# Optimization experiments

Hardware: AMD Instinct MI355X
Metric: run time of the kernel (lower is better)

## Reference

```python
import jax, jax.numpy as jnp
import numpy as np

C = 512
B, W, H = 16, 64, 64
K = 128


def setup_inputs() -> dict:
    key = jax.random.key(0)
    ks = jax.random.split(key, 17)
    s = 0.02
    inp = {
        "x1": jax.random.normal(ks[0], (B, C, W, H), jnp.float32),
        "y1": jax.random.normal(ks[1], (B, K, C), jnp.float32),
        "x2": jax.random.normal(ks[2], (B, C, W, H), jnp.float32),
        "y2": jax.random.normal(ks[3], (B, K, C), jnp.float32),
        # 1x1 conv weights stored as [out, in]
        "wq1": jax.random.normal(ks[4], (C // 4, C), jnp.float32) * s,
        "bq1": jnp.zeros((C // 4,), jnp.float32),
        "wq2": jax.random.normal(ks[5], (C // 4, C), jnp.float32) * s,
        "bq2": jnp.zeros((C // 4,), jnp.float32),
        "wk1": jax.random.normal(ks[6], (C // 2, C), jnp.float32) * s,
        "bk1": jnp.zeros((C // 2,), jnp.float32),
        "wk2": jax.random.normal(ks[7], (C // 2, C), jnp.float32) * s,
        "bk2": jnp.zeros((C // 2,), jnp.float32),
        "wv1": jax.random.normal(ks[8], (C, C), jnp.float32) * s,
        "bv1": jnp.zeros((C,), jnp.float32),
        "wv2": jax.random.normal(ks[9], (C, C), jnp.float32) * s,
        "bv2": jnp.zeros((C,), jnp.float32),
        "scale": jnp.ones((1,), jnp.float32) * 0.5,  # nn.Parameter(zeros) would kill grads; nonzero for testing
    }
    return inp


def reference(x1, y1, x2, y2, wq1, bq1, wq2, bq2, wk1, bk1, wk2, bk2,
              wv1, bv1, wv2, bv2, scale):
    b, c, w, h = x1.shape
    n = w * h
    # 1x1 convs == channel-wise linear maps
    q1 = jnp.einsum('bcwh,dc->bdwh', x1, wq1) + bq1[None, :, None, None]
    q2 = jnp.einsum('bcwh,dc->bdwh', x2, wq2) + bq2[None, :, None, None]
    # concat along channels -> [B, C/2, N] -> [B, N, C/2]
    q = jnp.concatenate([q1, q2], axis=1).reshape(b, c // 2, n).transpose(0, 2, 1)
    k1 = y1 @ wk1.T + bk1  # [B, K, C/2]
    k2 = y2 @ wk2.T + bk2
    v1 = y1 @ wv1.T + bv1  # [B, K, C]
    v2 = y2 @ wv2.T + bv2
    e1 = jnp.einsum('bnd,bkd->bnk', q, k1)  # [B, N, K]
    e2 = jnp.einsum('bnd,bkd->bnk', q, k2)
    attn = jax.nn.softmax(jnp.abs(e1 - e2), axis=-1)
    # out = value^T @ attn^T : [B, C, N]
    o1 = jnp.einsum('bkc,bnk->bcn', v1, attn).reshape(b, c, w, h)
    o2 = jnp.einsum('bkc,bnk->bcn', v2, attn).reshape(b, c, w, h)
    out1 = scale[0] * o1 + x1
    out2 = scale[0] * o2 + x2
    return out1, out2
```

## Files before the change

kernel.cpp:

```cpp
#include <hip/hip_runtime.h>

typedef unsigned short u16;
typedef __attribute__((ext_vector_type(8))) short short8v;
typedef __attribute__((ext_vector_type(4))) float floatx4;

#define B_ 16
#define C_ 512
#define N_ 4096
#define K_ 128

__device__ __forceinline__ float bf2f(u16 u) {
    unsigned int x = ((unsigned int)u) << 16;
    return __builtin_bit_cast(float, x);
}
__device__ __forceinline__ u16 f2bf(float f) {
    unsigned int u = __builtin_bit_cast(unsigned int, f);
    u = u + 0x7FFFu + ((u >> 16) & 1u);
    return (u16)(u >> 16);
}
__device__ __forceinline__ void gload_lds16(const u16* g, u16* l) {
    __builtin_amdgcn_global_load_lds(
        (const __attribute__((address_space(1))) void*)g,
        (__attribute__((address_space(3))) void*)l, 16, 0, 0);
}

__global__ void conv_all(const float* __restrict__ y1, const float* __restrict__ y2,
                         const float* __restrict__ wk1, const float* __restrict__ wk2,
                         const float* __restrict__ wv1, const float* __restrict__ wv2,
                         const float* __restrict__ wq1, const float* __restrict__ wq2,
                         u16* y1b, u16* y2b, u16* wk1b, u16* wk2b, u16* wv1b, u16* wv2b,
                         u16* wq1t, u16* wq2t) {
    int tid = blockIdx.x * 256 + threadIdx.x;
    const int SY = B_ * K_ * C_;
    const int SWK = 256 * 512;
    const int SWV = 512 * 512;
    const int SQ = 128 * 512;
    int base = 2*SY + 2*SWK + 2*SWV;
    if (tid < base) {
        const float* src; u16* dst; int off;
        if (tid < SY)                 { src = y1;  dst = y1b;  off = tid; }
        else if (tid < 2*SY)          { src = y2;  dst = y2b;  off = tid - SY; }
        else if (tid < 2*SY+SWK)      { src = wk1; dst = wk1b; off = tid - 2*SY; }
        else if (tid < 2*SY+2*SWK)    { src = wk2; dst = wk2b; off = tid - 2*SY - SWK; }
        else if (tid < 2*SY+2*SWK+SWV){ src = wv1; dst = wv1b; off = tid - 2*SY - 2*SWK; }
        else                          { src = wv2; dst = wv2b; off = tid - 2*SY - 2*SWK - SWV; }
        dst[off] = f2bf(src[off]);
    } else {
        int e = tid - base;
        const float* s = (e >= SQ) ? wq2 : wq1;
        u16* d = (e >= SQ) ? wq2t : wq1t;
        e &= (SQ - 1);
        int dd = e >> 9;
        int c = e & 511;
        d[c * 128 + dd] = f2bf(s[dd * 512 + c]);
    }
}

__global__ void gemm_gkgv(const u16* __restrict__ y1b, const u16* __restrict__ y2b,
                          const u16* __restrict__ wk1b, const u16* __restrict__ wk2b,
                          const u16* __restrict__ wv1b, const u16* __restrict__ wv2b,
                          const float* __restrict__ bk1, const float* __restrict__ bk2,
                          const float* __restrict__ bv1, const float* __restrict__ bv2,
                          u16* k1b, u16* k2b, u16* vt1, u16* vt2) {
    int l = threadIdx.x;
    int id = blockIdx.x;
    const u16 *A, *Bt; const float* bias; u16* outp;
    int m0, n0, po; bool bias_m;
    if (id < 256) {
        int bx = id & 1, by = (id >> 1) & 3, z = id >> 3;
        int b = z >> 1, which = z & 1;
        A = (which ? y2b : y1b) + (size_t)b * K_ * C_;
        Bt = which ? wk2b : wk1b;
        bias = which ? bk2 : bk1;
        outp = (which ? k2b : k1b) + (size_t)b * K_ * 256;
        m0 = bx * 64; n0 = by * 64; po = 256; bias_m = false;
    } else {
        int id2 = id - 256;
        int bx = id2 & 7, by = (id2 >> 3) & 1, z = id2 >> 4;
        int b = z >> 1, which = z & 1;
        A = which ? wv2b : wv1b;
        Bt = (which ? y2b : y1b) + (size_t)b * K_ * C_;
        bias = which ? bv2 : bv1;
        outp = (which ? vt2 : vt1) + (size_t)b * C_ * K_;
        m0 = bx * 64; n0 = by * 64; po = 128; bias_m = true;
    }
    floatx4 acc[4][4] = {};
    for (int ch = 0; ch < 16; ++ch) {
        int koff = ch * 32 + (l >> 4) * 8;
        short8v a[4], wv[4];
#pragma unroll
        for (int mf = 0; mf < 4; ++mf) a[mf] = *(const short8v*)(A + (size_t)(m0 + mf*16 + (l & 15)) * 512 + koff);
#pragma unroll
        for (int nf = 0; nf < 4; ++nf) wv[nf] = *(const short8v*)(Bt + (size_t)(n0 + nf*16 + (l & 15)) * 512 + koff);
#pragma unroll
        for (int mf = 0; mf < 4; ++mf)
#pragma unroll
            for (int nf = 0; nf < 4; ++nf)
                acc[mf][nf] = __builtin_amdgcn_mfma_f32_16x16x32_bf16(a[mf], wv[nf], acc[mf][nf], 0, 0, 0);
    }
#pragma unroll
    for (int mf = 0; mf < 4; ++mf)
#pragma unroll
        for (int nf = 0; nf < 4; ++nf)
#pragma unroll
            for (int rg = 0; rg < 4; ++rg) {
                int m = m0 + mf*16 + (l >> 4)*4 + rg;
                int n = n0 + nf*16 + (l & 15);
                outp[(size_t)m * po + n] = f2bf(acc[mf][nf][rg] + (bias_m ? bias[m] : bias[n]));
            }
}

__global__ void kd_sub(const u16* __restrict__ k1b, const u16* __restrict__ k2b,
                       u16* kd) {
    int tid = blockIdx.x * 256 + threadIdx.x;
    kd[tid] = f2bf(bf2f(k1b[tid]) - bf2f(k2b[tid]));
}

__global__ void ebd_k(const u16* __restrict__ kd,
                      const float* __restrict__ bq1, const float* __restrict__ bq2,
                      float* ebd) {
    int tid = blockIdx.x * 256 + threadIdx.x;
    const u16* kb = kd + (size_t)tid * 256;
    float s = 0.f;
    for (int d = 0; d < 128; ++d) s += bq1[d] * bf2f(kb[d]);
    for (int d = 0; d < 128; ++d) s += bq2[d] * bf2f(kb[128 + d]);
    ebd[tid] = s;
}

__global__ void gemm_gkk(const u16* __restrict__ kd,
                         const u16* __restrict__ wq1t, const u16* __restrict__ wq2t,
                         u16* kkd1, u16* kkd2) {
    int l = threadIdx.x;
    int z = blockIdx.z; int b = z >> 1; int which = z & 1;
    const u16* A = kd + (size_t)b * K_ * 256 + which * 128;
    const u16* Wt = which ? wq2t : wq1t;
    u16* outp = (which ? kkd2 : kkd1) + (size_t)b * K_ * C_;
    int m0 = blockIdx.x * 64, n0 = blockIdx.y * 64;
    floatx4 acc[4][4] = {};
    for (int ch = 0; ch < 4; ++ch) {
        int koff = ch * 32 + (l >> 4) * 8;
        short8v a[4], wv[4];
#pragma unroll
        for (int mf = 0; mf < 4; ++mf) a[mf] = *(const short8v*)(A + (size_t)(m0 + mf*16 + (l & 15)) * 256 + koff);
#pragma unroll
        for (int nf = 0; nf < 4; ++nf) wv[nf] = *(const short8v*)(Wt + (size_t)(n0 + nf*16 + (l & 15)) * 128 + koff);
#pragma unroll
        for (int mf = 0; mf < 4; ++mf)
#pragma unroll
            for (int nf = 0; nf < 4; ++nf)
                acc[mf][nf] = __builtin_amdgcn_mfma_f32_16x16x32_bf16(a[mf], wv[nf], acc[mf][nf], 0, 0, 0);
    }
#pragma unroll
    for (int mf = 0; mf < 4; ++mf)
#pragma unroll
        for (int nf = 0; nf < 4; ++nf)
#pragma unroll
            for (int rg = 0; rg < 4; ++rg) {
                int m = m0 + mf*16 + (l >> 4)*4 + rg;
                int n = n0 + nf*16 + (l & 15);
                outp[(size_t)m * C_ + n] = f2bf(acc[mf][nf][rg]);
            }
}

__global__ __launch_bounds__(256, 2)
void e_attn(const float* __restrict__ x1, const float* __restrict__ x2,
            const u16* __restrict__ kkd1, const u16* __restrict__ kkd2,
            const float* __restrict__ ebd, u16* __restrict__ attnb) {
    __shared__ u16 xT[2][128 * 64];
    __shared__ u16 kkS[2][128 * 64];

    int id = blockIdx.x;
    int sw = ((id & 7) << 6) | (id >> 3);
    int b = sw >> 5;
    int n0 = (sw & 31) * 128;
    int t = threadIdx.x, w = t >> 6, l = t & 63;

    const float* xs[2] = { x1 + (size_t)b * C_ * N_, x2 + (size_t)b * C_ * N_ };
    const u16* kkp[2] = { kkd1 + (size_t)b * K_ * C_, kkd2 + (size_t)b * K_ * C_ };

    floatx4 ed[2][8] = {};

    float xA0[16], xA1[16], xB0[16], xB1[16];

    auto SLOADX = [&](int s, float (&v0)[16], float (&v1)[16]) {
        int h = s >> 3, c0 = (s & 7) * 64;
        const float* xp = xs[h] + (size_t)(c0 + w * 16) * N_ + n0 + 2 * l;
#pragma unroll
        for (int j = 0; j < 16; ++j) {
            float2 f = *(const float2*)(xp + (size_t)j * N_);
            v0[j] = f.x; v1[j] = f.y;
        }
    };
    auto KLDS = [&](int s, int buf) {
        int h = s >> 3, c0 = (s & 7) * 64;
        const u16* kp = kkp[h] + c0;
#pragma unroll
        for (int i = 0; i < 4; ++i) {
            int gi = i * 256 + t;
            int key = gi >> 3, gp = gi & 7;
            gload_lds16(kp + (size_t)key * 512 + (gp ^ (key & 7)) * 8,
                        &kkS[buf][(i * 256 + w * 64) * 8]);
        }
    };
    auto SWRITEX = [&](int buf, float (&v0)[16], float (&v1)[16]) {
        short8v p00, p01, p10, p11;
#pragma unroll
        for (int j = 0; j < 8; ++j) {
            p00[j] = (short)f2bf(v0[j]);  p01[j] = (short)f2bf(v0[j + 8]);
            p10[j] = (short)f2bf(v1[j]);  p11[j] = (short)f2bf(v1[j + 8]);
        }
        u16* xb = xT[buf];
        int row0 = 2 * l, sz = l & 7;
        *(short8v*)&xb[row0 * 64 + 8 * ((w * 2) ^ sz)] = p00;
        *(short8v*)&xb[row0 * 64 + 8 * ((w * 2 + 1) ^ sz)] = p01;
        *(short8v*)&xb[(row0 + 1) * 64 + 8 * ((w * 2) ^ sz)] = p10;
        *(short8v*)&xb[(row0 + 1) * 64 + 8 * ((w * 2 + 1) ^ sz)] = p11;
    };
    auto COMPUTE = [&](int buf) {
        u16* xb = xT[buf]; u16* kb = kkS[buf];
#pragma unroll
        for (int cc = 0; cc < 2; ++cc) {
            short8v a[2];
#pragma unroll
            for (int mf = 0; mf < 2; ++mf) {
                int row = w * 32 + mf * 16 + (l & 15);
                int g = cc * 4 + (l >> 4);
                a[mf] = *(const short8v*)&xb[row * 64 + 8 * (g ^ ((row >> 1) & 7))];
            }
#pragma unroll
            for (int kf = 0; kf < 8; ++kf) {
                int key = kf * 16 + (l & 15);
                int g = cc * 4 + (l >> 4);
                short8v bb = *(const short8v*)&kb[key * 64 + 8 * (g ^ (key & 7))];
#pragma unroll
                for (int mf = 0; mf < 2; ++mf)
                    ed[mf][kf] = __builtin_amdgcn_mfma_f32_16x16x32_bf16(a[mf], bb, ed[mf][kf], 0, 0, 0);
            }
        }
    };

    SLOADX(0, xA0, xA1); KLDS(0, 0);
    SWRITEX(0, xA0, xA1);
    SLOADX(1, xB0, xB1); KLDS(1, 1);
#pragma unroll
    for (int rr = 0; rr < 8; ++rr) {
        int sA = 2 * rr, sB = 2 * rr + 1;
        __syncthreads();
        if (rr > 0) KLDS(sB, 1);
        COMPUTE(0);
        SWRITEX(1, xB0, xB1);
        if (sA + 2 <= 15) SLOADX(sA + 2, xA0, xA1);
        __syncthreads();
        if (sA + 2 <= 15) KLDS(sA + 2, 0);
        COMPUTE(1);
        if (sB + 1 <= 15) SWRITEX(0, xA0, xA1);
        if (sB + 2 <= 15) SLOADX(sB + 2, xB0, xB1);
    }

    float ebv[8];
#pragma unroll
    for (int kf = 0; kf < 8; ++kf) ebv[kf] = ebd[b * 128 + kf * 16 + (l & 15)];
#pragma unroll
    for (int mf = 0; mf < 2; ++mf)
#pragma unroll
        for (int kf = 0; kf < 8; ++kf)
#pragma unroll
            for (int rg = 0; rg < 4; ++rg)
                ed[mf][kf][rg] = fabsf(ed[mf][kf][rg] + ebv[kf]);

    float mx[2][4], sm[2][4];
#pragma unroll
    for (int mf = 0; mf < 2; ++mf)
#pragma unroll
        for (int rg = 0; rg < 4; ++rg) {
            float m = fmaxf(ed[mf][0][rg], ed[mf][1][rg]);
            m = fmaxf(m, fmaxf(ed[mf][2][rg], ed[mf][3][rg]));
            m = fmaxf(m, fmaxf(ed[mf][4][rg], ed[mf][5][rg]));
            m = fmaxf(m, fmaxf(ed[mf][6][rg], ed[mf][7][rg]));
            mx[mf][rg] = m;
        }
#pragma unroll
    for (int st = 1; st < 16; st <<= 1)
#pragma unroll
        for (int mf = 0; mf < 2; ++mf)
#pragma unroll
            for (int rg = 0; rg < 4; ++rg)
                mx[mf][rg] = fmaxf(mx[mf][rg], __shfl_xor(mx[mf][rg], st));
#pragma unroll
    for (int mf = 0; mf < 2; ++mf)
#pragma unroll
        for (int rg = 0; rg < 4; ++rg) sm[mf][rg] = 0.f;
#pragma unroll
    for (int mf = 0; mf < 2; ++mf)
#pragma unroll
        for (int kf = 0; kf < 8; ++kf)
#pragma unroll
            for (int rg = 0; rg < 4; ++rg) {
                float e = __expf(ed[mf][kf][rg] - mx[mf][rg]);
                ed[mf][kf][rg] = e;
                sm[mf][rg] += e;
            }
#pragma unroll
    for (int st = 1; st < 16; st <<= 1)
#pragma unroll
        for (int mf = 0; mf < 2; ++mf)
#pragma unroll
            for (int rg = 0; rg < 4; ++rg)
                sm[mf][rg] += __shfl_xor(sm[mf][rg], st);
#pragma unroll
    for (int mf = 0; mf < 2; ++mf)
#pragma unroll
        for (int rg = 0; rg < 4; ++rg) sm[mf][rg] = 1.0f / sm[mf][rg];

    u16* ap = attnb + ((size_t)(b * N_ + n0)) * 128;
#pragma unroll
    for (int mf = 0; mf < 2; ++mf)
#pragma unroll
        for (int rg = 0; rg < 4; ++rg) {
            int row = w * 32 + mf * 16 + (l >> 4) * 4 + rg;
#pragma unroll
            for (int kf = 0; kf < 8; ++kf) {
                int col = kf * 16 + (l & 15);
                ap[(size_t)row * 128 + col] = f2bf(ed[mf][kf][rg] * sm[mf][rg]);
            }
        }
}

__global__ __launch_bounds__(256, 2)
void pv_attn(const float* __restrict__ x1, const float* __restrict__ x2,
             const u16* __restrict__ vt1, const u16* __restrict__ vt2,
             const u16* __restrict__ attnb, const float* __restrict__ scale_p,
             float* __restrict__ out1, float* __restrict__ out2) {
    __shared__ u16 As[128 * 128];

    int id = blockIdx.x;
    int sw = ((id & 7) << 9) | (id >> 3);
    int b = sw >> 8;
    int ct = (sw >> 5) & 7;
    int pt = sw & 31;
    int n0 = pt * 128;
    int cb = ct * 128;
    int oi = cb >> 9;
    int cbl = cb & 511;
    int t = threadIdx.x, w = t >> 6, l = t & 63;

    const float sc = scale_p[0];
    const u16* vt = (oi ? vt2 : vt1) + (size_t)b * C_ * K_;
    const float* xr = (oi ? x2 : x1) + (size_t)b * C_ * N_;
    float* op = (oi ? out2 : out1) + (size_t)b * C_ * N_;

    const u16* ap = attnb + ((size_t)(b * N_ + n0)) * 128;
#pragma unroll
    for (int p = 0; p < 8; ++p) {
        int gi = p * 256 + t;
        int px = gi >> 4, gp = gi & 15;
        gload_lds16(ap + (size_t)px * 128 + (gp ^ (px & 15)) * 8,
                    &As[(p * 256 + w * 64) * 8]);
    }

    short8v vf[2][4];
#pragma unroll
    for (int mf = 0; mf < 2; ++mf)
#pragma unroll
        for (int kc = 0; kc < 4; ++kc)
            vf[mf][kc] = *(const short8v*)(vt + (size_t)(cbl + w * 32 + mf * 16 + (l & 15)) * K_ + kc * 32 + (l >> 4) * 8);

    float rs[2][4][8];
#pragma unroll
    for (int mf = 0; mf < 2; ++mf)
#pragma unroll
        for (int rg = 0; rg < 4; ++rg) {
            const float* rp = xr + (size_t)(cbl + w * 32 + mf * 16 + (l >> 4) * 4 + rg) * N_ + n0 + (l & 15);
#pragma unroll
            for (int nf = 0; nf < 8; ++nf)
                rs[mf][rg][nf] = rp[nf * 16];
        }
    __syncthreads();

    floatx4 o[2][8] = {};
#pragma unroll
    for (int kc = 0; kc < 4; ++kc) {
#pragma unroll
        for (int nf = 0; nf < 8; ++nf) {
            int row = nf * 16 + (l & 15);
            int g = kc * 4 + (l >> 4);
            short8v bb = *(const short8v*)&As[row * 128 + 8 * (g ^ (row & 15))];
#pragma unroll
            for (int mf = 0; mf < 2; ++mf)
                o[mf][nf] = __builtin_amdgcn_mfma_f32_16x16x32_bf16(vf[mf][kc], bb, o[mf][nf], 0, 0, 0);
        }
    }

#pragma unroll
    for (int mf = 0; mf < 2; ++mf)
#pragma unroll
        for (int rg = 0; rg < 4; ++rg) {
            float* wp = op + (size_t)(cbl + w * 32 + mf * 16 + (l >> 4) * 4 + rg) * N_ + n0 + (l & 15);
#pragma unroll
            for (int nf = 0; nf < 8; ++nf)
                wp[nf * 16] = sc * o[mf][nf][rg] + rs[mf][rg][nf];
        }
}

extern "C" void kernel_launch(void* const* d_in, const int* in_sizes, int n_in,
                              void* d_out, int out_size, void* d_ws, size_t ws_size,
                              hipStream_t stream) {
    const float* x1 = (const float*)d_in[0];
    const float* y1 = (const float*)d_in[1];
    const float* x2 = (const float*)d_in[2];
    const float* y2 = (const float*)d_in[3];
    const float* wq1 = (const float*)d_in[4];
    const float* bq1 = (const float*)d_in[5];
    const float* wq2 = (const float*)d_in[6];
    const float* bq2 = (const float*)d_in[7];
    const float* wk1 = (const float*)d_in[8];
    const float* bk1 = (const float*)d_in[9];
    const float* wk2 = (const float*)d_in[10];
    const float* bk2 = (const float*)d_in[11];
    const float* wv1 = (const float*)d_in[12];
    const float* bv1 = (const float*)d_in[13];
    const float* wv2 = (const float*)d_in[14];
    const float* bv2 = (const float*)d_in[15];
    const float* scale = (const float*)d_in[16];

    char* ws = (char*)d_ws;
    u16* y1b  = (u16*)(ws + 0);
    u16* y2b  = (u16*)(ws + 2097152);
    u16* wk1b = (u16*)(ws + 4194304);
    u16* wk2b = (u16*)(ws + 4456448);
    u16* wv1b = (u16*)(ws + 4718592);
    u16* wv2b = (u16*)(ws + 5242880);
    u16* wq1t = (u16*)(ws + 5767168);
    u16* wq2t = (u16*)(ws + 5898240);
    u16* k1b  = (u16*)(ws + 6029312);
    u16* k2b  = (u16*)(ws + 7077888);
    u16* kd   = (u16*)(ws + 8126464);
    u16* kkd1 = (u16*)(ws + 9175040);
    u16* kkd2 = (u16*)(ws + 11272192);
    u16* vt1  = (u16*)(ws + 13369344);
    u16* vt2  = (u16*)(ws + 15466496);
    float* ebd = (float*)(ws + 17563648);
    u16* attnb = (u16*)(ws + 17571840);

    float* out1 = (float*)d_out;
    float* out2 = out1 + (size_t)B_ * C_ * N_;

    hipLaunchKernelGGL(conv_all, dim3(11776), dim3(256), 0, stream,
                       y1, y2, wk1, wk2, wv1, wv2, wq1, wq2,
                       y1b, y2b, wk1b, wk2b, wv1b, wv2b, wq1t, wq2t);
    hipLaunchKernelGGL(gemm_gkgv, dim3(768), dim3(64), 0, stream,
                       y1b, y2b, wk1b, wk2b, wv1b, wv2b, bk1, bk2, bv1, bv2,
                       k1b, k2b, vt1, vt2);
    hipLaunchKernelGGL(kd_sub, dim3(2048), dim3(256), 0, stream, k1b, k2b, kd);
    hipLaunchKernelGGL(ebd_k, dim3(8), dim3(256), 0, stream, kd, bq1, bq2, ebd);
    hipLaunchKernelGGL(gemm_gkk, dim3(2, 8, 32), dim3(64), 0, stream,
                       kd, wq1t, wq2t, kkd1, kkd2);
    hipLaunchKernelGGL(e_attn, dim3(512), dim3(256), 0, stream,
                       x1, x2, kkd1, kkd2, ebd, attnb);
    hipLaunchKernelGGL(pv_attn, dim3(4096), dim3(256), 0, stream,
                       x1, x2, vt1, vt2, attnb, scale, out1, out2);
}
```

Measured before the change: 232.2 us.

## Fuse score/softmax and PV attention kernels, keeping attention tile in LDS

Merges the score/softmax kernel with the attention-times-value kernel. Each block now writes its normalized attention tile into shared memory (reusing the key-staging buffer) and loops over all 8 channel chunks of both outputs, double-buffering the V fragment loads. This removes the bf16 attention round trip through global memory and one kernel launch. In exchange the grid drops from 4096 to 512 blocks, so each block does 8 times more PV work with less parallelism to hide memory latency on the x reads and output writes.

```diff
diff --git a/kernel.cpp b/kernel.cpp
--- a/kernel.cpp
+++ b/kernel.cpp
@@ -163,11 +163,15 @@
 }
 
 __global__ __launch_bounds__(256, 2)
-void e_attn(const float* __restrict__ x1, const float* __restrict__ x2,
-            const u16* __restrict__ kkd1, const u16* __restrict__ kkd2,
-            const float* __restrict__ ebd, u16* __restrict__ attnb) {
-    __shared__ u16 xT[2][128 * 64];
-    __shared__ u16 kkS[2][128 * 64];
+void fused_attn(const float* __restrict__ x1, const float* __restrict__ x2,
+                const u16* __restrict__ kkd1, const u16* __restrict__ kkd2,
+                const u16* __restrict__ vt1, const u16* __restrict__ vt2,
+                const float* __restrict__ ebd, const float* __restrict__ scale_p,
+                float* __restrict__ out1, float* __restrict__ out2) {
+    __shared__ u16 smem[32768];
+    u16* xT[2]  = { smem,         smem + 8192 };
+    u16* kkS[2] = { smem + 16384, smem + 24576 };
+    u16* attn_s = smem + 16384;
 
     int id = blockIdx.x;
     int sw = ((id & 7) << 6) | (id >> 3);
@@ -312,7 +316,7 @@
 #pragma unroll
         for (int rg = 0; rg < 4; ++rg) sm[mf][rg] = 1.0f / sm[mf][rg];
 
-    u16* ap = attnb + ((size_t)(b * N_ + n0)) * 128;
+    __syncthreads();
 #pragma unroll
     for (int mf = 0; mf < 2; ++mf)
 #pragma unroll
@@ -321,85 +325,63 @@
 #pragma unroll
             for (int kf = 0; kf < 8; ++kf) {
                 int col = kf * 16 + (l & 15);
-                ap[(size_t)row * 128 + col] = f2bf(ed[mf][kf][rg] * sm[mf][rg]);
-            }
-        }
-}
-
-__global__ __launch_bounds__(256, 2)
-void pv_attn(const float* __restrict__ x1, const float* __restrict__ x2,
-             const u16* __restrict__ vt1, const u16* __restrict__ vt2,
-             const u16* __restrict__ attnb, const float* __restrict__ scale_p,
-             float* __restrict__ out1, float* __restrict__ out2) {
-    __shared__ u16 As[128 * 128];
-
-    int id = blockIdx.x;
-    int sw = ((id & 7) << 9) | (id >> 3);
-    int b = sw >> 8;
-    int ct = (sw >> 5) & 7;
-    int pt = sw & 31;
-    int n0 = pt * 128;
-    int cb = ct * 128;
-    int oi = cb >> 9;
-    int cbl = cb & 511;
-    int t = threadIdx.x, w = t >> 6, l = t & 63;
+                attn_s[row * 128 + 8 * ((col >> 3) ^ (row & 15)) + (col & 7)] =
+                    f2bf(ed[mf][kf][rg] * sm[mf][rg]);
+            }
+        }
+    __syncthreads();
 
     const float sc = scale_p[0];
-    const u16* vt = (oi ? vt2 : vt1) + (size_t)b * C_ * K_;
-    const float* xr = (oi ? x2 : x1) + (size_t)b * C_ * N_;
-    float* op = (oi ? out2 : out1) + (size_t)b * C_ * N_;
-
-    const u16* ap = attnb + ((size_t)(b * N_ + n0)) * 128;
-#pragma unroll
-    for (int p = 0; p < 8; ++p) {
-        int gi = p * 256 + t;
-        int px = gi >> 4, gp = gi & 15;
-        gload_lds16(ap + (size_t)px * 128 + (gp ^ (px & 15)) * 8,
-                    &As[(p * 256 + w * 64) * 8]);
-    }
-
-    short8v vf[2][4];
-#pragma unroll
-    for (int mf = 0; mf < 2; ++mf)
-#pragma unroll
-        for (int kc = 0; kc < 4; ++kc)
-            vf[mf][kc] = *(const short8v*)(vt + (size_t)(cbl + w * 32 + mf * 16 + (l & 15)) * K_ + kc * 32 + (l >> 4) * 8);
-
-    float rs[2][4][8];
-#pragma unroll
-    for (int mf = 0; mf < 2; ++mf)
-#pragma unroll
-        for (int rg = 0; rg < 4; ++rg) {
-            const float* rp = xr + (size_t)(cbl + w * 32 + mf * 16 + (l >> 4) * 4 + rg) * N_ + n0 + (l & 15);
-#pragma unroll
-            for (int nf = 0; nf < 8; ++nf)
-                rs[mf][rg][nf] = rp[nf * 16];
-        }
-    __syncthreads();
-
-    floatx4 o[2][8] = {};
-#pragma unroll
-    for (int kc = 0; kc < 4; ++kc) {
-#pragma unroll
-        for (int nf = 0; nf < 8; ++nf) {
-            int row = nf * 16 + (l & 15);
-            int g = kc * 4 + (l >> 4);
-            short8v bb = *(const short8v*)&As[row * 128 + 8 * (g ^ (row & 15))];
-#pragma unroll
-            for (int mf = 0; mf < 2; ++mf)
-                o[mf][nf] = __builtin_amdgcn_mfma_f32_16x16x32_bf16(vf[mf][kc], bb, o[mf][nf], 0, 0, 0);
-        }
-    }
-
-#pragma unroll
-    for (int mf = 0; mf < 2; ++mf)
-#pragma unroll
-        for (int rg = 0; rg < 4; ++rg) {
-            float* wp = op + (size_t)(cbl + w * 32 + mf * 16 + (l >> 4) * 4 + rg) * N_ + n0 + (l & 15);
-#pragma unroll
-            for (int nf = 0; nf < 8; ++nf)
-                wp[nf * 16] = sc * o[mf][nf][rg] + rs[mf][rg][nf];
-        }
+    const u16* vts[2] = { vt1 + (size_t)b * C_ * K_, vt2 + (size_t)b * C_ * K_ };
+    float* outs[2] = { out1 + (size_t)b * C_ * N_, out2 + (size_t)b * C_ * N_ };
+
+    short8v vfA[2][4], vfB[2][4];
+    auto LOADVF = [&](int s, short8v (&vf)[2][4]) {
+        int oi = s >> 2, cc = s & 3;
+        const u16* vt = vts[oi];
+#pragma unroll
+        for (int mf = 0; mf < 2; ++mf)
+#pragma unroll
+            for (int kc = 0; kc < 4; ++kc)
+                vf[mf][kc] = *(const short8v*)(vt + (size_t)(cc * 128 + w * 32 + mf * 16 + (l & 15)) * K_ + kc * 32 + (l >> 4) * 8);
+    };
+    auto COMPPV = [&](int s, short8v (&vf)[2][4]) {
+        int oi = s >> 2, cc = s & 3;
+        const float* xr = xs[oi];
+        float* op = outs[oi];
+        floatx4 o[2][8] = {};
+#pragma unroll
+        for (int kc = 0; kc < 4; ++kc) {
+#pragma unroll
+            for (int nf = 0; nf < 8; ++nf) {
+                int row = nf * 16 + (l & 15);
+                int g = kc * 4 + (l >> 4);
+                short8v bb = *(const short8v*)&attn_s[row * 128 + 8 * (g ^ (row & 15))];
+#pragma unroll
+                for (int mf = 0; mf < 2; ++mf)
+                    o[mf][nf] = __builtin_amdgcn_mfma_f32_16x16x32_bf16(vf[mf][kc], bb, o[mf][nf], 0, 0, 0);
+            }
+        }
+#pragma unroll
+        for (int mf = 0; mf < 2; ++mf)
+#pragma unroll
+            for (int rg = 0; rg < 4; ++rg) {
+                size_t rowoff = (size_t)(cc * 128 + w * 32 + mf * 16 + (l >> 4) * 4 + rg) * N_ + n0 + (l & 15);
+#pragma unroll
+                for (int nf = 0; nf < 8; ++nf)
+                    op[rowoff + nf * 16] = sc * o[mf][nf][rg] + xr[rowoff + nf * 16];
+            }
+    };
+
+    LOADVF(0, vfA);
+    LOADVF(1, vfB);
+#pragma unroll
+    for (int ss = 0; ss < 4; ++ss) {
+        COMPPV(2 * ss, vfA);
+        if (2 * ss + 2 < 8) LOADVF(2 * ss + 2, vfA);
+        COMPPV(2 * ss + 1, vfB);
+        if (2 * ss + 3 < 8) LOADVF(2 * ss + 3, vfB);
+    }
 }
 
 extern "C" void kernel_launch(void* const* d_in, const int* in_sizes, int n_in,
@@ -440,7 +422,6 @@
     u16* vt1  = (u16*)(ws + 13369344);
     u16* vt2  = (u16*)(ws + 15466496);
     float* ebd = (float*)(ws + 17563648);
-    u16* attnb = (u16*)(ws + 17571840);
 
     float* out1 = (float*)d_out;
     float* out2 = out1 + (size_t)B_ * C_ * N_;
@@ -455,8 +436,6 @@
     hipLaunchKernelGGL(ebd_k, dim3(8), dim3(256), 0, stream, kd, bq1, bq2, ebd);
     hipLaunchKernelGGL(gemm_gkk, dim3(2, 8, 32), dim3(64), 0, stream,
                        kd, wq1t, wq2t, kkd1, kkd2);
-    hipLaunchKernelGGL(e_attn, dim3(512), dim3(256), 0, stream,
-                       x1, x2, kkd1, kkd2, ebd, attnb);
-    hipLaunchKernelGGL(pv_attn, dim3(4096), dim3(256), 0, stream,
-                       x1, x2, vt1, vt2, attnb, scale, out1, out2);
-}
+    hipLaunchKernelGGL(fused_attn, dim3(512), dim3(256), 0, stream,
+                       x1, x2, kkd1, kkd2, vt1, vt2, ebd, scale, out1, out2);
+}
```

New measurement: 449.3 us. +93.5%, slower.

## Halve e_attn position tile to 64 and double grid for more parallelism

Applied to the files above, without the earlier changes.

The e_attn kernel now handles 64 spatial positions per block instead of 128, so the grid doubles from 512 to 1024 blocks and each wave computes one 16-row MFMA fragment instead of two. Register use drops (half the accumulators and staging registers), launch bounds allow 3 blocks per CU, and shared memory shrinks to 48 KB. The aim is better occupancy and load balance across the CUs for this memory-bound phase, at the cost of loading the full 128x512 kkd tile twice as often per position.

```diff
diff --git a/kernel.cpp b/kernel.cpp
--- a/kernel.cpp
+++ b/kernel.cpp
@@ -162,34 +162,45 @@
             }
 }
 
-__global__ __launch_bounds__(256, 2)
+__global__ __launch_bounds__(256, 3)
 void e_attn(const float* __restrict__ x1, const float* __restrict__ x2,
             const u16* __restrict__ kkd1, const u16* __restrict__ kkd2,
             const float* __restrict__ ebd, u16* __restrict__ attnb) {
-    __shared__ u16 xT[2][128 * 64];
-    __shared__ u16 kkS[2][128 * 64];
+    __shared__ u16 smem[24576];
+    u16* xT[2]  = { smem,         smem + 4096 };
+    u16* kkS[2] = { smem + 8192,  smem + 16384 };
 
     int id = blockIdx.x;
-    int sw = ((id & 7) << 6) | (id >> 3);
-    int b = sw >> 5;
-    int n0 = (sw & 31) * 128;
+    int sw = ((id & 7) << 7) | (id >> 3);
+    int b = sw >> 6;
+    int n0 = (sw & 63) * 64;
     int t = threadIdx.x, w = t >> 6, l = t & 63;
 
     const float* xs[2] = { x1 + (size_t)b * C_ * N_, x2 + (size_t)b * C_ * N_ };
     const u16* kkp[2] = { kkd1 + (size_t)b * K_ * C_, kkd2 + (size_t)b * K_ * C_ };
 
-    floatx4 ed[2][8] = {};
-
-    float xA0[16], xA1[16], xB0[16], xB1[16];
-
-    auto SLOADX = [&](int s, float (&v0)[16], float (&v1)[16]) {
+    floatx4 ed[8] = {};
+
+    float xA0[8], xA1[8], xB0[8], xB1[8];
+
+    auto SLOADX = [&](int s, float (&v0)[8], float (&v1)[8]) {
         int h = s >> 3, c0 = (s & 7) * 64;
-        const float* xp = xs[h] + (size_t)(c0 + w * 16) * N_ + n0 + 2 * l;
-#pragma unroll
-        for (int j = 0; j < 16; ++j) {
+        const float* xp = xs[h] + (size_t)(c0 + w * 16 + (l >> 5) * 8) * N_ + n0 + 2 * (l & 31);
+#pragma unroll
+        for (int j = 0; j < 8; ++j) {
             float2 f = *(const float2*)(xp + (size_t)j * N_);
             v0[j] = f.x; v1[j] = f.y;
         }
+    };
+    auto SWRITEX = [&](int buf, float (&v0)[8], float (&v1)[8]) {
+        short8v p0, p1;
+#pragma unroll
+        for (int j = 0; j < 8; ++j) { p0[j] = (short)f2bf(v0[j]); p1[j] = (short)f2bf(v1[j]); }
+        u16* xb = xT[buf];
+        int row0 = 2 * (l & 31);
+        int szz = 8 * ((w * 2 + (l >> 5)) ^ ((l & 31) & 7));
+        *(short8v*)&xb[row0 * 64 + szz] = p0;
+        *(short8v*)&xb[(row0 + 1) * 64 + szz] = p1;
     };
     auto KLDS = [&](int s, int buf) {
         int h = s >> 3, c0 = (s & 7) * 64;
@@ -202,39 +213,18 @@
                         &kkS[buf][(i * 256 + w * 64) * 8]);
         }
     };
-    auto SWRITEX = [&](int buf, float (&v0)[16], float (&v1)[16]) {
-        short8v p00, p01, p10, p11;
-#pragma unroll
-        for (int j = 0; j < 8; ++j) {
-            p00[j] = (short)f2bf(v0[j]);  p01[j] = (short)f2bf(v0[j + 8]);
-            p10[j] = (short)f2bf(v1[j]);  p11[j] = (short)f2bf(v1[j + 8]);
-        }
-        u16* xb = xT[buf];
-        int row0 = 2 * l, sz = l & 7;
-        *(short8v*)&xb[row0 * 64 + 8 * ((w * 2) ^ sz)] = p00;
-        *(short8v*)&xb[row0 * 64 + 8 * ((w * 2 + 1) ^ sz)] = p01;
-        *(short8v*)&xb[(row0 + 1) * 64 + 8 * ((w * 2) ^ sz)] = p10;
-        *(short8v*)&xb[(row0 + 1) * 64 + 8 * ((w * 2 + 1) ^ sz)] = p11;
-    };
     auto COMPUTE = [&](int buf) {
         u16* xb = xT[buf]; u16* kb = kkS[buf];
 #pragma unroll
         for (int cc = 0; cc < 2; ++cc) {
-            short8v a[2];
-#pragma unroll
-            for (int mf = 0; mf < 2; ++mf) {
-                int row = w * 32 + mf * 16 + (l & 15);
-                int g = cc * 4 + (l >> 4);
-                a[mf] = *(const short8v*)&xb[row * 64 + 8 * (g ^ ((row >> 1) & 7))];
-            }
+            int g = cc * 4 + (l >> 4);
+            int row = w * 16 + (l & 15);
+            short8v a = *(const short8v*)&xb[row * 64 + 8 * (g ^ ((row >> 1) & 7))];
 #pragma unroll
             for (int kf = 0; kf < 8; ++kf) {
                 int key = kf * 16 + (l & 15);
-                int g = cc * 4 + (l >> 4);
                 short8v bb = *(const short8v*)&kb[key * 64 + 8 * (g ^ (key & 7))];
-#pragma unroll
-                for (int mf = 0; mf < 2; ++mf)
-                    ed[mf][kf] = __builtin_amdgcn_mfma_f32_16x16x32_bf16(a[mf], bb, ed[mf][kf], 0, 0, 0);
+                ed[kf] = __builtin_amdgcn_mfma_f32_16x16x32_bf16(a, bb, ed[kf], 0, 0, 0);
             }
         }
     };
@@ -261,69 +251,53 @@
 #pragma unroll
     for (int kf = 0; kf < 8; ++kf) ebv[kf] = ebd[b * 128 + kf * 16 + (l & 15)];
 #pragma unroll
-    for (int mf = 0; mf < 2; ++mf)
-#pragma unroll
-        for (int kf = 0; kf < 8; ++kf)
-#pragma unroll
-            for (int rg = 0; rg < 4; ++rg)
-                ed[mf][kf][rg] = fabsf(ed[mf][kf][rg] + ebv[kf]);
-
-    float mx[2][4], sm[2][4];
-#pragma unroll
-    for (int mf = 0; mf < 2; ++mf)
+    for (int kf = 0; kf < 8; ++kf)
+#pragma unroll
+        for (int rg = 0; rg < 4; ++rg)
+            ed[kf][rg] = fabsf(ed[kf][rg] + ebv[kf]);
+
+    float m4[4];
+#pragma unroll
+    for (int rg = 0; rg < 4; ++rg) {
+        float m = fmaxf(ed[0][rg], ed[1][rg]);
+        m = fmaxf(m, fmaxf(ed[2][rg], ed[3][rg]));
+        m = fmaxf(m, fmaxf(ed[4][rg], ed[5][rg]));
+        m = fmaxf(m, fmaxf(ed[6][rg], ed[7][rg]));
+        m4[rg] = m;
+    }
+#pragma unroll
+    for (int st = 1; st < 16; st <<= 1)
+#pragma unroll
+        for (int rg = 0; rg < 4; ++rg)
+            m4[rg] = fmaxf(m4[rg], __shfl_xor(m4[rg], st));
+
+    float s4[4] = {0.f, 0.f, 0.f, 0.f};
+#pragma unroll
+    for (int kf = 0; kf < 8; ++kf)
 #pragma unroll
         for (int rg = 0; rg < 4; ++rg) {
-            float m = fmaxf(ed[mf][0][rg], ed[mf][1][rg]);
-            m = fmaxf(m, fmaxf(ed[mf][2][rg], ed[mf][3][rg]));
-            m = fmaxf(m, fmaxf(ed[mf][4][rg], ed[mf][5][rg]));
-            m = fmaxf(m, fmaxf(ed[mf][6][rg], ed[mf][7][rg]));
-            mx[mf][rg] = m;
+            float e = __expf(ed[kf][rg] - m4[rg]);
+            ed[kf][rg] = e;
+            s4[rg] += e;
         }
 #pragma unroll
     for (int st = 1; st < 16; st <<= 1)
 #pragma unroll
-        for (int mf = 0; mf < 2; ++mf)
-#pragma unroll
-            for (int rg = 0; rg < 4; ++rg)
-                mx[mf][rg] = fmaxf(mx[mf][rg], __shfl_xor(mx[mf][rg], st));
-#pragma unroll
-    for (int mf = 0; mf < 2; ++mf)
-#pragma unroll
-        for (int rg = 0; rg < 4; ++rg) sm[mf][rg] = 0.f;
-#pragma unroll
-    for (int mf = 0; mf < 2; ++mf)
-#pragma unroll
-        for (int kf = 0; kf < 8; ++kf)
-#pragma unroll
-            for (int rg = 0; rg < 4; ++rg) {
-                float e = __expf(ed[mf][kf][rg] - mx[mf][rg]);
-                ed[mf][kf][rg] = e;
-                sm[mf][rg] += e;
-            }
-#pragma unroll
-    for (int st = 1; st < 16; st <<= 1)
-#pragma unroll
-        for (int mf = 0; mf < 2; ++mf)
-#pragma unroll
-            for (int rg = 0; rg < 4; ++rg)
-                sm[mf][rg] += __shfl_xor(sm[mf][rg], st);
-#pragma unroll
-    for (int mf = 0; mf < 2; ++mf)
-#pragma unroll
-        for (int rg = 0; rg < 4; ++rg) sm[mf][rg] = 1.0f / sm[mf][rg];
+        for (int rg = 0; rg < 4; ++rg)
+            s4[rg] += __shfl_xor(s4[rg], st);
+#pragma unroll
+    for (int rg = 0; rg < 4; ++rg) s4[rg] = 1.0f / s4[rg];
 
     u16* ap = attnb + ((size_t)(b * N_ + n0)) * 128;
 #pragma unroll
-    for (int mf = 0; mf < 2; ++mf)
-#pragma unroll
-        for (int rg = 0; rg < 4; ++rg) {
-            int row = w * 32 + mf * 16 + (l >> 4) * 4 + rg;
-#pragma unroll
-            for (int kf = 0; kf < 8; ++kf) {
-                int col = kf * 16 + (l & 15);
-                ap[(size_t)row * 128 + col] = f2bf(ed[mf][kf][rg] * sm[mf][rg]);
-            }
-        }
+    for (int rg = 0; rg < 4; ++rg) {
+        int row = w * 16 + (l >> 4) * 4 + rg;
+#pragma unroll
+        for (int kf = 0; kf < 8; ++kf) {
+            int col = kf * 16 + (l & 15);
+            ap[(size_t)row * 128 + col] = f2bf(ed[kf][rg] * s4[rg]);
+        }
+    }
 }
 
 __global__ __launch_bounds__(256, 2)
@@ -455,7 +429,7 @@
     hipLaunchKernelGGL(ebd_k, dim3(8), dim3(256), 0, stream, kd, bq1, bq2, ebd);
     hipLaunchKernelGGL(gemm_gkk, dim3(2, 8, 32), dim3(64), 0, stream,
                        kd, wq1t, wq2t, kkd1, kkd2);
-    hipLaunchKernelGGL(e_attn, dim3(512), dim3(256), 0, stream,
+    hipLaunchKernelGGL(e_attn, dim3(1024), dim3(256), 0, stream,
                        x1, x2, kkd1, kkd2, ebd, attnb);
     hipLaunchKernelGGL(pv_attn, dim3(4096), dim3(256), 0, stream,
                        x1, x2, vt1, vt2, attnb, scale, out1, out2);
```

Result: slower. 246.8 us (+6.3%).

## Deepen e_attn x-load pipeline to three register stages with explicit vmcnt barriers

Applied to the files above, without the earlier changes.

Restructures the e_attn main loop so global loads of x run two stages ahead using three register buffers instead of two. Each stage now ends in a single barrier that waits on a partial vmcnt, in place of two full __syncthreads. sched_barrier fences stop the compiler from reordering across stages. The aim is to hide global-load latency behind MFMA compute, at the cost of more register pressure, which under launch_bounds(256,2) risks spilling. The hand-counted vmcnt values must also exactly match the in-flight loads for the code to stay correct.

```diff
diff --git a/kernel.cpp b/kernel.cpp
--- a/kernel.cpp
+++ b/kernel.cpp
@@ -23,6 +23,12 @@
         (const __attribute__((address_space(1))) void*)g,
         (__attribute__((address_space(3))) void*)l, 16, 0, 0);
 }
+
+#define BARRIER_VM(VMC) do { \
+    asm volatile("s_waitcnt vmcnt(" #VMC ") lgkmcnt(0)" ::: "memory"); \
+    __builtin_amdgcn_s_barrier(); \
+    __builtin_amdgcn_sched_barrier(0); \
+} while (0)
 
 __global__ void conv_all(const float* __restrict__ y1, const float* __restrict__ y2,
                          const float* __restrict__ wk1, const float* __restrict__ wk2,
@@ -180,7 +186,7 @@
 
     floatx4 ed[2][8] = {};
 
-    float xA0[16], xA1[16], xB0[16], xB1[16];
+    float xv0_0[16], xv1_0[16], xv0_1[16], xv1_1[16], xv0_2[16], xv1_2[16];
 
     auto SLOADX = [&](int s, float (&v0)[16], float (&v1)[16]) {
         int h = s >> 3, c0 = (s & 7) * 64;
@@ -239,23 +245,35 @@
         }
     };
 
-    SLOADX(0, xA0, xA1); KLDS(0, 0);
-    SWRITEX(0, xA0, xA1);
-    SLOADX(1, xB0, xB1); KLDS(1, 1);
-#pragma unroll
-    for (int rr = 0; rr < 8; ++rr) {
-        int sA = 2 * rr, sB = 2 * rr + 1;
-        __syncthreads();
-        if (rr > 0) KLDS(sB, 1);
-        COMPUTE(0);
-        SWRITEX(1, xB0, xB1);
-        if (sA + 2 <= 15) SLOADX(sA + 2, xA0, xA1);
-        __syncthreads();
-        if (sA + 2 <= 15) KLDS(sA + 2, 0);
-        COMPUTE(1);
-        if (sB + 1 <= 15) SWRITEX(0, xA0, xA1);
-        if (sB + 2 <= 15) SLOADX(sB + 2, xB0, xB1);
-    }
+#define REGION(S, XW0, XW1, XL0, XL1, DO_W, DO_L, VMC) do { \
+        if ((S) + 1 <= 15) KLDS((S) + 1, ((S) + 1) & 1); \
+        __builtin_amdgcn_sched_barrier(0); \
+        COMPUTE((S) & 1); \
+        if (DO_W) SWRITEX(((S) + 1) & 1, XW0, XW1); \
+        if (DO_L) SLOADX((S) + 3, XL0, XL1); \
+        BARRIER_VM(VMC); \
+    } while (0)
+
+    SLOADX(0, xv0_0, xv1_0);
+    KLDS(0, 0);
+    __builtin_amdgcn_sched_barrier(0);
+    SLOADX(1, xv0_1, xv1_1);
+    SLOADX(2, xv0_2, xv1_2);
+    SWRITEX(0, xv0_0, xv1_0);
+    BARRIER_VM(32);
+
+#pragma unroll
+    for (int k3 = 0; k3 < 4; ++k3) {
+        int s0 = k3 * 3;
+        REGION(s0 + 0, xv0_1, xv1_1, xv0_0, xv1_0, 1, 1, 16);
+        REGION(s0 + 1, xv0_2, xv1_2, xv0_1, xv1_1, 1, 1, 16);
+        REGION(s0 + 2, xv0_0, xv1_0, xv0_2, xv1_2, 1, 1, 16);
+    }
+    REGION(12, xv0_1, xv1_1, xv0_0, xv1_0, 1, 1, 16);
+    REGION(13, xv0_2, xv1_2, xv0_0, xv1_0, 1, 0, 0);
+    REGION(14, xv0_0, xv1_0, xv0_0, xv1_0, 1, 0, 0);
+    COMPUTE(15 & 1);
+#undef REGION
 
     float ebv[8];
 #pragma unroll
```

Measured after the change: 232.7 us. About the same (+0.2%).
